# Performance work log

Hardware: AMD Instinct MI355X
Metric: run time of the kernel (lower is better)

The kernel has to match this reference:

```python
import jax, jax.numpy as jnp
import numpy as np

A_LO = 0      # interval lower bound
B_HI = 63     # interval upper bound -> window W = 64
PAD_BIG = 1.0e4  # finite pad so exp(-scale*PAD_BIG) == 0 exactly in fp32 (no inf/nan grads)


def setup_inputs() -> dict:
    key = jax.random.key(0)
    k1, k2 = jax.random.split(key)
    B, T = 64, 2048
    phi = jax.random.normal(k1, (B, T, 2), dtype=jnp.float32)
    psi = jax.random.normal(k2, (B, T, 2), dtype=jnp.float32)
    return {"phi": phi, "psi": psi, "scale": 8}


def reference(phi, psi, scale):
    # phi, psi: [B, T, 2] robustness traces of left/right subformulas.
    a, b = A_LO, B_HI
    Bsz, T, _ = phi.shape
    W = b - a + 1
    s = jnp.float32(scale)

    # Pad time axis so every window of length W fits. phi padded with a large
    # value (neutral for smooth-min), psi with a large negative value (neutral
    # for smooth-max); both exactly neutral in fp32 since exp(-s*1e4) == 0.
    phi_pad = jnp.pad(phi, ((0, 0), (0, b), (0, 0)), constant_values=PAD_BIG)
    psi_pad = jnp.pad(psi, ((0, 0), (0, b), (0, 0)), constant_values=-PAD_BIG)

    # tau = t + a + j, j in [0, W)
    idx = jnp.arange(T)[:, None] + jnp.arange(a, b + 1)[None, :]  # [T, W]
    phi_win = phi_pad[:, idx]  # [B, T, W, 2], phi at t+k
    psi_win = psi_pad[:, idx]  # [B, T, W, 2], psi at tau

    # Smooth min over phi[t : tau] (exclusive of tau):
    #   min_phi(k) = -logsumexp_{s'=t..t+k-1}(-s*phi[s']) / s
    # computed via a cumulative logsumexp over the window axis.
    neg = -s * phi_win
    cumlse = jax.lax.associative_scan(jnp.logaddexp, neg, axis=2)  # [B,T,W,2]
    shifted = jnp.concatenate(
        [jnp.zeros_like(cumlse[:, :, :1]), cumlse[:, :, :-1]], axis=2)
    k_off = jnp.arange(W)[None, None, :, None] + a  # tau - t
    # tau == t -> min over empty segment -> ones (per original code)
    min_phi = jnp.where(k_off == 0, jnp.float32(1.0), -shifted / s)

    # Smooth min of the pair {min_phi, psi[tau]}
    cand = -jnp.logaddexp(-s * min_phi, -s * psi_win) / s  # [B,T,W,2]

    # Mask tau > T-1 (candidates that don't exist in the original loop).
    valid = (jnp.arange(T)[:, None] + a + jnp.arange(W)[None, :]) <= (T - 1)
    cand = jnp.where(valid[None, :, :, None], cand, -PAD_BIG)

    # Smooth max over candidate taus
    best = jax.nn.logsumexp(s * cand, axis=2) / s  # [B, T, 2]
    return best
```

## Files before the change

### kernel.cpp

```cpp
#include <hip/hip_runtime.h>
#include <math.h>


#define T_DIM   2048
#define W_WIN   64
#define BLOCK_T 256
#define STAGE   (BLOCK_T + W_WIN - 1)

__global__ __launch_bounds__(BLOCK_T) void until_kernel(
    const float* __restrict__ phi,
    const float* __restrict__ psi,
    const int*  __restrict__ scale_p,
    float* __restrict__ out)
{
    __shared__ float4 s_d[STAGE];

    const int b   = blockIdx.y;
    const int t0  = blockIdx.x * BLOCK_T;
    const int tid = threadIdx.x;
    const float s  = (float)(*scale_p);
    const float ns = -s;

    const float2* __restrict__ phi2 = (const float2*)(phi + (size_t)b * T_DIM * 2);
    const float2* __restrict__ psi2 = (const float2*)(psi + (size_t)b * T_DIM * 2);

    for (int i = tid; i < STAGE; i += BLOCK_T) {
        int t = t0 + i;
        float4 v;
        if (t < T_DIM) {
            float2 pv = phi2[t];
            float2 qv = psi2[t];
            v.x = __expf(ns * pv.x);
            v.y = __expf(ns * pv.y);
            v.z = __expf(ns * qv.x);
            v.w = __expf(ns * qv.y);
        } else {
            v.x = 0.f; v.y = 0.f;
            v.z = INFINITY; v.w = INFINITY;
        }
        s_d[i] = v;
    }
    __syncthreads();

    const float Es = __expf(ns);

    float4 v0 = s_d[tid];
    float accA0 = __builtin_amdgcn_rcpf(Es + v0.z);
    float accA1 = __builtin_amdgcn_rcpf(Es + v0.w);
    float accB0 = 0.f, accB1 = 0.f;
    float sum0 = v0.x;
    float sum1 = v0.y;

    #pragma unroll
    for (int k = 1; k < W_WIN; ++k) {
        float4 v = s_d[tid + k];
        float r0 = __builtin_amdgcn_rcpf(sum0 + v.z);
        float r1 = __builtin_amdgcn_rcpf(sum1 + v.w);
        if (k & 1) { accA0 += r0; accA1 += r1; }
        else       { accB0 += r0; accB1 += r1; }
        sum0 += v.x;
        sum1 += v.y;
    }

    const int t = t0 + tid;
    float2* __restrict__ out2 = (float2*)(out + (size_t)b * T_DIM * 2);
    out2[t] = make_float2(__logf(accA0 + accB0) / s, __logf(accA1 + accB1) / s);
}

extern "C" void kernel_launch(void* const* d_in, const int* in_sizes, int n_in,
                              void* d_out, int out_size, void* d_ws, size_t ws_size,
                              hipStream_t stream) {
    const float* phi   = (const float*)d_in[0];
    const float* psi   = (const float*)d_in[1];
    const int*   scale = (const int*)d_in[2];
    float* out = (float*)d_out;

    const int B = in_sizes[0] / (T_DIM * 2);
    dim3 grid(T_DIM / BLOCK_T, B);
    until_kernel<<<grid, dim3(BLOCK_T), 0, stream>>>(phi, psi, scale, out);
}
```

Baseline: 61.28 us.

## Split each output's 64-step window across 8 threads with shared-memory prefix sums

Each output time step now uses eight threads, each covering an 8-element chunk of the window instead of one thread walking all 64 steps. Chunk sums are exchanged through shared memory to form exclusive prefix sums, and partial reciprocal sums are reduced by one thread per output. This shortens the serial dependency chain per thread and increases parallelism. The cost is more threads, extra shared-memory traffic and three block barriers, with output tiles shrinking to 64 per block.

After: 62.98 us. 2.8% more time.

```diff
diff --git a/kernel.cpp b/kernel.cpp
--- a/kernel.cpp
+++ b/kernel.cpp
@@ -4,30 +4,36 @@
 
 #define T_DIM   2048
 #define W_WIN   64
-#define BLOCK_T 256
-#define STAGE   (BLOCK_T + W_WIN - 1)
+#define OUT_T   64
+#define NW      8
+#define NTHR    (OUT_T * NW)
+#define STAGE   (OUT_T + W_WIN - 1)
+#define KPL     (W_WIN / NW)
 
-__global__ __launch_bounds__(BLOCK_T) void until_kernel(
+__global__ __launch_bounds__(NTHR, 4) void until_kernel(
     const float* __restrict__ phi,
     const float* __restrict__ psi,
     const int*  __restrict__ scale_p,
     float* __restrict__ out)
 {
     __shared__ float4 s_d[STAGE];
+    __shared__ float2 s_g[OUT_T][NW];
+    __shared__ float2 s_r[OUT_T][NW];
 
     const int b   = blockIdx.y;
-    const int t0  = blockIdx.x * BLOCK_T;
+    const int t0  = blockIdx.x * OUT_T;
     const int tid = threadIdx.x;
+    const int o   = tid & 63;
+    const int j   = tid >> 6;
     const float s  = (float)(*scale_p);
     const float ns = -s;
 
-    const float2* __restrict__ phi2 = (const float2*)(phi + (size_t)b * T_DIM * 2);
-    const float2* __restrict__ psi2 = (const float2*)(psi + (size_t)b * T_DIM * 2);
-
-    for (int i = tid; i < STAGE; i += BLOCK_T) {
-        int t = t0 + i;
+    if (tid < STAGE) {
+        const int t = t0 + tid;
         float4 v;
         if (t < T_DIM) {
+            const float2* __restrict__ phi2 = (const float2*)(phi + (size_t)b * T_DIM * 2);
+            const float2* __restrict__ psi2 = (const float2*)(psi + (size_t)b * T_DIM * 2);
             float2 pv = phi2[t];
             float2 qv = psi2[t];
             v.x = __expf(ns * pv.x);
@@ -35,36 +41,67 @@
             v.z = __expf(ns * qv.x);
             v.w = __expf(ns * qv.y);
         } else {
-            v.x = 0.f; v.y = 0.f;
+            v.x = 0.f;      v.y = 0.f;
             v.z = INFINITY; v.w = INFINITY;
         }
-        s_d[i] = v;
+        s_d[tid] = v;
     }
     __syncthreads();
 
+    const float4* __restrict__ sp = s_d + o + KPL * j;
+    float4 v[KPL];
+    #pragma unroll
+    for (int i = 0; i < KPL; ++i) v[i] = sp[i];
+
+    float g0 = 0.f, g1 = 0.f;
+    #pragma unroll
+    for (int i = 0; i < KPL; ++i) { g0 += v[i].x; g1 += v[i].y; }
+    s_g[o][j] = make_float2(g0, g1);
+    __syncthreads();
+
+    float sum0 = 0.f, sum1 = 0.f;
+    #pragma unroll
+    for (int m = 0; m < NW - 1; ++m) {
+        const float2 gm = s_g[o][m];
+        if (m < j) { sum0 += gm.x; sum1 += gm.y; }
+    }
+
     const float Es = __expf(ns);
 
-    float4 v0 = s_d[tid];
-    float accA0 = __builtin_amdgcn_rcpf(Es + v0.z);
-    float accA1 = __builtin_amdgcn_rcpf(Es + v0.w);
-    float accB0 = 0.f, accB1 = 0.f;
-    float sum0 = v0.x;
-    float sum1 = v0.y;
+    float accA0, accA1, accB0 = 0.f, accB1 = 0.f;
 
+    {
+        const float b0 = (j == 0) ? Es : sum0;
+        const float b1 = (j == 0) ? Es : sum1;
+        accA0 = __builtin_amdgcn_rcpf(b0 + v[0].z);
+        accA1 = __builtin_amdgcn_rcpf(b1 + v[0].w);
+        sum0 += v[0].x;
+        sum1 += v[0].y;
+    }
     #pragma unroll
-    for (int k = 1; k < W_WIN; ++k) {
-        float4 v = s_d[tid + k];
-        float r0 = __builtin_amdgcn_rcpf(sum0 + v.z);
-        float r1 = __builtin_amdgcn_rcpf(sum1 + v.w);
-        if (k & 1) { accA0 += r0; accA1 += r1; }
-        else       { accB0 += r0; accB1 += r1; }
-        sum0 += v.x;
-        sum1 += v.y;
+    for (int i = 1; i < KPL; ++i) {
+        const float r0 = __builtin_amdgcn_rcpf(sum0 + v[i].z);
+        const float r1 = __builtin_amdgcn_rcpf(sum1 + v[i].w);
+        if (i & 1) { accB0 += r0; accB1 += r1; }
+        else       { accA0 += r0; accA1 += r1; }
+        sum0 += v[i].x;
+        sum1 += v[i].y;
     }
 
-    const int t = t0 + tid;
-    float2* __restrict__ out2 = (float2*)(out + (size_t)b * T_DIM * 2);
-    out2[t] = make_float2(__logf(accA0 + accB0) / s, __logf(accA1 + accB1) / s);
+    s_r[o][j] = make_float2(accA0 + accB0, accA1 + accB1);
+    __syncthreads();
+
+    if (j == 0) {
+        float a0 = 0.f, a1 = 0.f;
+        #pragma unroll
+        for (int m = 0; m < NW; ++m) {
+            const float2 rm = s_r[o][m];
+            a0 += rm.x;
+            a1 += rm.y;
+        }
+        float2* __restrict__ out2 = (float2*)(out + (size_t)b * T_DIM * 2);
+        out2[t0 + o] = make_float2(__logf(a0) / s, __logf(a1) / s);
+    }
 }
 
 extern "C" void kernel_launch(void* const* d_in, const int* in_sizes, int n_in,
@@ -76,6 +113,6 @@
     float* out = (float*)d_out;
 
     const int B = in_sizes[0] / (T_DIM * 2);
-    dim3 grid(T_DIM / BLOCK_T, B);
-    until_kernel<<<grid, dim3(BLOCK_T), 0, stream>>>(phi, psi, scale, out);
+    dim3 grid(T_DIM / OUT_T, B);
+    until_kernel<<<grid, dim3(NTHR), 0, stream>>>(phi, psi, scale, out);
 }
```
